# Optimization experiments

Hardware: AMD Instinct MI355X
Metric: run time of the kernel (lower is better)

Reference implementation:

```python
import jax, jax.numpy as jnp
import numpy as np

C = jnp.complex64

def _ry_mat(t):
    c = jnp.cos(t / 2).astype(C)
    s = jnp.sin(t / 2).astype(C)
    return jnp.stack([jnp.stack([c, -s], -1), jnp.stack([s, c], -1)], -2)

def _rx_mat(t):
    c = jnp.cos(t / 2).astype(C)
    s = (-1j) * jnp.sin(t / 2).astype(C)
    return jnp.stack([jnp.stack([c, s], -1), jnp.stack([s, c], -1)], -2)

def _rz_mat(t):
    em = jnp.exp(-1j * (t / 2).astype(C))
    ep = jnp.exp(1j * (t / 2).astype(C))
    z = jnp.zeros_like(em)
    return jnp.stack([jnp.stack([em, z], -1), jnp.stack([z, ep], -1)], -2)

def _apply_1q(psi, gate, w):
    # psi: [bsz, 2^n]; gate: [2,2] (shared) or [bsz,2,2] (per-sample)
    bsz = psi.shape[0]
    s = psi.reshape(bsz, 1 << w, 2, -1)  # wire w isolated on axis 2
    if gate.ndim == 2:
        out = jnp.einsum('ij,bljr->blir', gate, s)
    else:
        out = jnp.einsum('bij,bljr->blir', gate, s)
    return out.reshape(bsz, -1)

def _apply_cnot(psi, c, t):
    bsz = psi.shape[0]
    a, b = min(c, t), max(c, t)
    s = psi.reshape(bsz, 1 << a, 2, 1 << (b - a - 1), 2, -1)
    if c < t:
        # control on axis 2, target on axis 4; after slicing ctrl=1, target -> axis 3
        s = s.at[:, :, 1].set(jnp.flip(s[:, :, 1], axis=3))
    else:
        # control on axis 4, target on axis 2
        s = s.at[:, :, :, :, 1].set(jnp.flip(s[:, :, :, :, 1], axis=2))
    return s.reshape(bsz, -1)

def setup_inputs() -> dict:
    key = jax.random.key(0)
    k1, k2 = jax.random.split(key)
    bsz, n_wires, n_qlayers = 1024, 14, 4
    x_raw = jax.random.normal(k1, (bsz, n_wires), dtype=jnp.float32)
    angles = jax.random.normal(k2, (n_qlayers, n_wires, 3), dtype=jnp.float32) * 0.1
    return {"x_raw": x_raw, "angles": angles}

def reference(x_raw, angles):
    L, n, _ = angles.shape
    bsz = x_raw.shape[0]
    x_enc = jnp.tanh(x_raw[:, :n]) * jnp.pi  # [bsz, n]
    # |0...0> statevector, wire 0 is the most significant bit
    psi = jnp.zeros((bsz, 1 << n), dtype=C).at[:, 0].set(1.0)
    # RY encoding (per-sample angles)
    for w in range(n):
        psi = _apply_1q(psi, _ry_mat(x_enc[:, w]), w)
    # variational layers
    for k in range(L):
        for w in range(n):
            psi = _apply_1q(psi, _rx_mat(angles[k, w, 0]), w)
            psi = _apply_1q(psi, _ry_mat(angles[k, w, 1]), w)
            psi = _apply_1q(psi, _rz_mat(angles[k, w, 2]), w)
        for i in range(n - 1):
            psi = _apply_cnot(psi, i, i + 1)
        psi = _apply_cnot(psi, n - 1, 0)
    # <Z_0>: +|amp|^2 when bit0=0, -|amp|^2 when bit0=1
    p = jnp.abs(psi.reshape(bsz, 2, -1)) ** 2
    return (p[:, 0].sum(-1) - p[:, 1].sum(-1)).astype(jnp.float32)
```

## Files before the change

### kernel.cpp

```cpp
#include <hip/hip_runtime.h>
#include <cmath>
#include <cstdint>

#define NW       14
#define NST      (1 << NW)
#define THREADS  512
#define PRETHR   768
#define NPASS    12
#define WTP      512

typedef _Float16 f16;
typedef _Float16 f16x8 __attribute__((ext_vector_type(8)));
typedef float    f32x4 __attribute__((ext_vector_type(4)));
typedef unsigned short u16;

struct PassArg { u16 Mm[4]; u16 Mt[3]; u16 Mw[3]; };
struct Plan { PassArg ps[NPASS]; u16 initM[14]; u16 measR; u16 _pad; };

__device__ __forceinline__ float2 cmulf(float2 a, float2 b) {
    return make_float2(a.x * b.x - a.y * b.y, a.x * b.y + a.y * b.x);
}
__device__ __host__ __forceinline__ unsigned wtofs(unsigned m, unsigned q01) {
    return (m * 16 + q01 * 8) ^ (((m >> 2) & 1u) << 3);
}

__global__ __launch_bounds__(PRETHR)
void vqc_pre(const float* __restrict__ angles, f16* __restrict__ wt_g,
             float2* __restrict__ u0_g)
{
    __shared__ float2 G[4 * NW * 4];
    const int tid = threadIdx.x;

    if (tid < 4 * NW) {
        const int k = tid / NW, w = tid % NW;
        const float a  = angles[(k * NW + w) * 3 + 0];
        const float bb = angles[(k * NW + w) * 3 + 1];
        const float c  = angles[(k * NW + w) * 3 + 2];
        float sa, ca, sb, cb, sc, cc;
        sincosf(a * 0.5f, &sa, &ca);
        sincosf(bb * 0.5f, &sb, &cb);
        sincosf(c * 0.5f, &sc, &cc);
        float2 m00 = make_float2(cb * ca,  sb * sa);
        float2 m01 = make_float2(-sb * ca, -cb * sa);
        float2 m10 = make_float2(sb * ca,  -cb * sa);
        float2 m11 = make_float2(cb * ca,  -sb * sa);
        const float2 e0 = make_float2(cc, -sc), e1 = make_float2(cc, sc);
        const float2 u00 = cmulf(e0, m00), u01 = cmulf(e0, m01);
        const float2 u10 = cmulf(e1, m10), u11 = cmulf(e1, m11);
        const int gi = (k * NW + w) * 4;
        G[gi + 0] = u00; G[gi + 1] = u01; G[gi + 2] = u10; G[gi + 3] = u11;
        if (k == 0) {
            u0_g[w * 4 + 0] = u00; u0_g[w * 4 + 1] = u01;
            u0_g[w * 4 + 2] = u10; u0_g[w * 4 + 3] = u11;
        }
    }
    __syncthreads();

    {
        const int p = tid >> 6, l6 = tid & 63;
        const int ap = l6 & 15, ahalf = (l6 >> 4) & 1, dup = l6 >> 5;
        const int layer = (p >> 2) + 1, g = p & 3;

        float2 p3;
        if (g == 3) {
            p3 = make_float2((((ap >> 3) & 1) == ahalf) ? 1.f : 0.f, 0.f);
        } else {
            const int wire = 13 - (10 - 4 * g + 3);
            p3 = G[(layer * NW + wire) * 4 + ((ap >> 3) & 1) * 2 + ahalf];
        }
        float2 e0a, e0b, e1a, e1b, e2a, e2b;
        {
            const int r0 = ap & 1, r1 = (ap >> 1) & 1, r2 = (ap >> 2) & 1;
            if (g == 3) {
                const float2* G13 = G + (layer * NW + 13) * 4;
                const float2* G12 = G + (layer * NW + 12) * 4;
                e0a = G13[r0 * 2 + 0]; e0b = G13[r0 * 2 + 1];
                e1a = G12[r1 * 2 + 0]; e1b = G12[r1 * 2 + 1];
                e2a = make_float2(r2 == 0 ? 1.f : 0.f, 0.f);
                e2b = make_float2(r2 == 1 ? 1.f : 0.f, 0.f);
            } else {
                const float2* G0 = G + (layer * NW + (13 - (10 - 4 * g + 0))) * 4;
                const float2* G1 = G + (layer * NW + (13 - (10 - 4 * g + 1))) * 4;
                const float2* G2 = G + (layer * NW + (13 - (10 - 4 * g + 2))) * 4;
                e0a = G0[r0 * 2 + 0]; e0b = G0[r0 * 2 + 1];
                e1a = G1[r1 * 2 + 0]; e1b = G1[r1 * 2 + 1];
                e2a = G2[r2 * 2 + 0]; e2b = G2[r2 * 2 + 1];
            }
        }
        f16x8 frag;
        #pragma unroll
        for (int j2 = 0; j2 < 8; ++j2) {
            float2 v = cmulf(p3, (j2 & 4) ? e2b : e2a);
            v = cmulf(v, (j2 & 2) ? e1b : e1a);
            v = cmulf(v, (j2 & 1) ? e0b : e0a);
            frag[j2] = (f16)(dup ? v.y : v.x);
        }
        *(f16x8*)(wt_g + p * WTP + dup * 256 + wtofs(ap, ahalf)) = frag;
    }
}

__global__ __launch_bounds__(THREADS, 4)
void vqc_kernel(const float* __restrict__ x_raw, const f16* __restrict__ wt_g,
                const float2* __restrict__ u0_g, float* __restrict__ out, Plan pl)
{
    extern __shared__ char smem[];
    f16*    Sh  = (f16*)smem;
    f16*    Wt  = Sh + 2 * NST;
    float2* G0c = (float2*)(Wt + NPASS * WTP);
    float*  red = (float*)(G0c + 2 * NW);

    const int b   = blockIdx.x;
    const int tid = threadIdx.x;
    const int lane = tid & 63, wv = tid >> 6;
    const int q = lane >> 4, m = lane & 15;

    {
        const uint4* src = (const uint4*)wt_g;
        uint4* dst = (uint4*)Wt;
        dst[tid] = src[tid];
        if (tid < 256) dst[512 + tid] = src[512 + tid];
    }
    if (tid < NW) {
        const float xe = tanhf(x_raw[b * NW + tid]) * 3.14159265358979f;
        float se, ce;
        sincosf(xe * 0.5f, &se, &ce);
        const float2 u00 = u0_g[tid * 4 + 0], u01 = u0_g[tid * 4 + 1];
        const float2 u10 = u0_g[tid * 4 + 2], u11 = u0_g[tid * 4 + 3];
        G0c[tid * 2 + 0] = make_float2(u00.x * ce + u01.x * se, u00.y * ce + u01.y * se);
        G0c[tid * 2 + 1] = make_float2(u10.x * ce + u11.x * se, u10.y * ce + u11.y * se);
    }
    __syncthreads();

    {
        float2 common = make_float2(1.f, 0.f);
        #pragma unroll
        for (int bit = 0; bit < 9; ++bit) {
            const int w = 13 - bit;
            const float2 f = ((tid >> bit) & 1) ? G0c[w * 2 + 1] : G0c[w * 2 + 0];
            common = cmulf(common, f);
        }
        unsigned p9 = 0;
        #pragma unroll
        for (int bit = 0; bit < 9; ++bit)
            p9 ^= ((tid >> bit) & 1) ? (unsigned)pl.initM[bit] : 0u;

        const float2 f0a = G0c[4*2+0], f0b = G0c[4*2+1];
        const float2 f1a = G0c[3*2+0], f1b = G0c[3*2+1];
        const float2 f2a = G0c[2*2+0], f2b = G0c[2*2+1];
        const float2 f3a = G0c[1*2+0], f3b = G0c[1*2+1];
        const float2 f4a = G0c[0*2+0], f4b = G0c[0*2+1];

        const unsigned S   = (unsigned)pl.initM[13];
        const unsigned Slo = S & 15u, Hh = S & ~15u;
        const unsigned plo = p9 & 15u, B0 = p9 & ~15u;

        #pragma unroll
        for (int c = 0; c < 2; ++c) {
            const unsigned r = plo ^ (c ? Slo : 0u);
            const bool s0 = ((r       ) & 1u) != 0;
            const bool s1 = (((r) ^ (r >> 1)) & 1u) != 0;
            const bool s2 = (((r >> 1) ^ (r >> 2)) & 1u) != 0;
            const bool s3 = (((r >> 2) ^ (r >> 3)) & 1u) != 0;
            const bool s4 = ((((r >> 3) & 1u) ^ (unsigned)c) != 0);
            const float2 F0[2] = { s0 ? f0b : f0a, s0 ? f0a : f0b };
            const float2 F1[2] = { s1 ? f1b : f1a, s1 ? f1a : f1b };
            const float2 F2[2] = { s2 ? f2b : f2a, s2 ? f2a : f2b };
            const float2 F3[2] = { s3 ? f3b : f3a, s3 ? f3a : f3b };
            const float2 F4[2] = { s4 ? f4b : f4a, s4 ? f4a : f4b };
            const float2 A0 = cmulf(common, F4[0]);
            const float2 A1 = cmulf(common, F4[1]);
            float2 Bt[4];
            Bt[0] = cmulf(A0, F3[0]); Bt[1] = cmulf(A0, F3[1]);
            Bt[2] = cmulf(A1, F3[1]); Bt[3] = cmulf(A1, F3[0]);
            float2 Ct[8];
            #pragma unroll
            for (int o32 = 0; o32 < 4; ++o32) {
                const int o2 = o32 & 1;
                Ct[o32 * 2 + 0] = cmulf(Bt[o32], F2[o2]);
                Ct[o32 * 2 + 1] = cmulf(Bt[o32], F2[1 ^ o2]);
            }
            float2 Gt[4];
            Gt[0] = cmulf(F1[0], F0[0]); Gt[1] = cmulf(F1[1], F0[1]);
            Gt[2] = cmulf(F1[1], F0[0]); Gt[3] = cmulf(F1[0], F0[1]);

            union { f16 h[8]; f16x8 v; } hR[2], hI[2];
            #pragma unroll
            for (int o = 0; o < 16; ++o) {
                const int o0 = o & 1, o1 = (o >> 1) & 1;
                const float2 amp = cmulf(Ct[o >> 1], Gt[o1 * 2 + o0]);
                hR[o >> 3].h[o & 7] = (f16)amp.x;
                hI[o >> 3].h[o & 7] = (f16)amp.y;
            }
            const unsigned bb = B0 ^ (c ? Hh : 0u);
            *(f16x8*)(Sh + bb)           = hR[0].v;
            *(f16x8*)(Sh + bb + 8)       = hR[1].v;
            *(f16x8*)(Sh + NST + bb)     = hI[0].v;
            *(f16x8*)(Sh + NST + bb + 8) = hI[1].v;
        }
    }
    __syncthreads();

    const unsigned plane_off = (unsigned)(q >> 1) << 14;
    const unsigned q01 = (unsigned)(q & 1);
    const f32x4 z4 = {0.f, 0.f, 0.f, 0.f};
    #pragma unroll
    for (int p = 0; p < NPASS; ++p) {
        const PassArg& P = pl.ps[p];
        const unsigned pm = ((m & 1) ? P.Mm[0] : 0) ^ ((m & 2) ? P.Mm[1] : 0)
                          ^ ((m & 4) ? P.Mm[2] : 0) ^ ((m & 8) ? P.Mm[3] : 0);
        const unsigned wb = ((wv & 1) ? P.Mw[0] : 0) ^ ((wv & 2) ? P.Mw[1] : 0)
                          ^ ((wv & 4) ? P.Mw[2] : 0);
        const unsigned b0 = pm ^ wb;
        const f16x8 tr = *(const f16x8*)(Wt + p * WTP +       wtofs((unsigned)m, q01));
        const f16x8 ti = *(const f16x8*)(Wt + p * WTP + 256 + wtofs((unsigned)m, q01));
        const f16x8 bf1 = (q < 2) ? tr : -ti;
        const f16x8 bf2 = (q < 2) ? ti : tr;
        unsigned sw[8];
        f16x8 av[8];
        #pragma unroll
        for (int tt = 0; tt < 8; ++tt) {
            sw[tt] = b0 ^ ((tt & 1) ? P.Mt[0] : 0)
                        ^ ((tt & 2) ? P.Mt[1] : 0)
                        ^ ((tt & 4) ? P.Mt[2] : 0);
            av[tt] = *(const f16x8*)(Sh + plane_off + (sw[tt] ^ (q01 << 3)));
        }
        #pragma unroll
        for (int tt = 0; tt < 8; ++tt) {
            const f32x4 d1 = __builtin_amdgcn_mfma_f32_16x16x32_f16(av[tt], bf1, z4, 0, 0, 0);
            const f32x4 d2 = __builtin_amdgcn_mfma_f32_16x16x32_f16(av[tt], bf2, z4, 0, 0, 0);
            union { f16 h[4]; uint2 u; } c1, c2;
            #pragma unroll
            for (int r = 0; r < 4; ++r) { c1.h[r] = (f16)d1[r]; c2.h[r] = (f16)d2[r]; }
            const unsigned wu = sw[tt] ^ ((unsigned)q << 2);
            *(uint2*)(Sh + wu)       = c1.u;
            *(uint2*)(Sh + NST + wu) = c2.u;
        }
        __syncthreads();
    }

    float acc = 0.f;
    {
        #pragma unroll
        for (int cch = 0; cch < 4; ++cch) {
            const unsigned addr = (unsigned)cch * 4096u + (unsigned)tid * 8u;
            const f16x8 rr = *(const f16x8*)(Sh + addr);
            const f16x8 ii = *(const f16x8*)(Sh + NST + addr);
            const int pb = __popc(addr & (unsigned)pl.measR) & 1;
            #pragma unroll
            for (int e = 0; e < 8; ++e) {
                const float re = (float)rr[e], im = (float)ii[e];
                const float pw = fmaf(re, re, im * im);
                const int sgn = pb ^ (__popc((unsigned)e & (unsigned)pl.measR) & 1);
                acc += sgn ? -pw : pw;
            }
        }
    }
    #pragma unroll
    for (int off = 32; off > 0; off >>= 1) acc += __shfl_down(acc, off);
    if ((tid & 63) == 0) red[wv] = acc;
    __syncthreads();
    if (tid == 0) {
        float s = 0.f;
        #pragma unroll
        for (int i = 0; i < THREADS / 64; ++i) s += red[i];
        out[b] = s;
    }
}

struct GFm { u16 col[14]; };

static unsigned ringp_host(unsigned x) {
    unsigned s = x;
    s ^= s >> 1; s ^= s >> 2; s ^= s >> 4; s ^= s >> 8;
    s &= 0x3FFFu;
    return (s ^ ((s & 1u) << 13)) & 0x3FFFu;
}
static u16 gf_apply(const GFm& m, u16 v) {
    u16 r = 0;
    for (int b = 0; b < 14; ++b) if ((v >> b) & 1) r ^= m.col[b];
    return r;
}
static GFm gf_compose(const GFm& A, const GFm& B) {
    GFm C;
    for (int b = 0; b < 14; ++b) C.col[b] = gf_apply(A, B.col[b]);
    return C;
}
static void rows_from(const GFm& A, u16 r[14]) {
    for (int i = 0; i < 14; ++i) {
        u16 mm = 0;
        for (int b = 0; b < 14; ++b) mm |= (u16)(((A.col[b] >> i) & 1) << b);
        r[i] = mm;
    }
}
static GFm from_rows(const u16 r[14]) {
    GFm A;
    for (int b = 0; b < 14; ++b) {
        u16 c = 0;
        for (int i = 0; i < 14; ++i) c |= (u16)(((r[i] >> b) & 1) << i);
        A.col[b] = c;
    }
    return A;
}
static GFm gf_inv(const GFm& A) {
    u16 M[14], I[14];
    rows_from(A, M);
    for (int i = 0; i < 14; ++i) I[i] = (u16)(1u << i);
    for (int c = 0; c < 14; ++c) {
        int p = c;
        while (p < 14 && !((M[p] >> c) & 1)) ++p;
        if (p == 14) continue;
        u16 t = M[c]; M[c] = M[p]; M[p] = t;
        t = I[c]; I[c] = I[p]; I[p] = t;
        for (int r2 = 0; r2 < 14; ++r2)
            if (r2 != c && ((M[r2] >> c) & 1)) { M[r2] ^= M[c]; I[r2] ^= I[c]; }
    }
    return from_rows(I);
}

static void build_plan(Plan& pl) {
    GFm ring, ringInv;
    for (int b = 0; b < 14; ++b) ring.col[b] = (u16)ringp_host(1u << b);
    ringInv = gf_inv(ring);

    GFm phi;
    for (int j = 0; j < 4; ++j) phi.col[10 + j] = (u16)(1u << j);
    for (int j = 0; j < 4; ++j) phi.col[6 + j]  = (u16)(1u << (4 + j));
    for (int j = 0; j < 4; ++j) phi.col[2 + j]  = (u16)(1u << (8 + j));
    phi.col[0] = (u16)(1u << 12);
    phi.col[1] = (u16)(1u << 13);

    for (int b = 0; b < 14; ++b) pl.initM[b] = gf_apply(phi, ring.col[b]);

    const int gb[4][4] = {{10,11,12,13},{6,7,8,9},{2,3,4,5},{0,1,6,7}};

    for (int p = 0; p < NPASS; ++p) {
        const int g = p & 3;
        u16 uv[4];
        if (g < 3) for (int j = 0; j < 4; ++j) uv[j] = (u16)(1u << gb[g + 1][j]);
        else       for (int j = 0; j < 4; ++j) uv[j] = ringInv.col[10 + j];
        for (int j = 0; j < 4; ++j) pl.ps[p].Mm[j] = gf_apply(phi, uv[j]);

        u16 span[14]; int ns = 0;
        u16 tv[6]; int nt = 0;
        auto tryAdd = [&](u16 v) -> bool {
            bool ch = true;
            while (ch) {
                ch = false;
                for (int i = 0; i < ns; ++i) {
                    const int tb = 31 - __builtin_clz((unsigned)span[i]);
                    if ((v >> tb) & 1) { v ^= span[i]; ch = true; }
                }
            }
            if (!v) return false;
            span[ns++] = v;
            return true;
        };
        for (int j = 0; j < 4; ++j) tryAdd((u16)(1u << gb[g][j]));
        for (int j = 0; j < 4; ++j) tryAdd(uv[j]);
        for (int b2 = 0; b2 < 14 && nt < 6; ++b2)
            if (tryAdd((u16)(1u << b2))) tv[nt++] = (u16)(1u << b2);
        for (int i = 0; i < 3; ++i) pl.ps[p].Mt[i] = gf_apply(phi, tv[i]);
        for (int i = 0; i < 3; ++i) pl.ps[p].Mw[i] = gf_apply(phi, tv[i + 3]);

        GFm Bm;
        for (int j = 0; j < 4; ++j) Bm.col[j]     = (u16)(1u << gb[g][j]);
        for (int j = 0; j < 4; ++j) Bm.col[4 + j] = uv[j];
        for (int i = 0; i < 6; ++i) Bm.col[8 + i] = tv[i];
        GFm Binv = gf_inv(Bm);
        u16 img[14];
        for (int j = 0; j < 4; ++j) img[j]     = pl.ps[p].Mm[j];
        for (int j = 0; j < 4; ++j) img[4 + j] = (u16)(1u << j);
        for (int i = 0; i < 6; ++i) img[8 + i] = gf_apply(phi, tv[i]);
        GFm nphi;
        for (int b2 = 0; b2 < 14; ++b2) {
            const u16 coef = gf_apply(Binv, (u16)(1u << b2));
            u16 v = 0;
            for (int j = 0; j < 14; ++j) if ((coef >> j) & 1) v ^= img[j];
            nphi.col[b2] = v;
        }
        if (g == 3) nphi = gf_compose(nphi, ringInv);
        phi = nphi;
    }

    GFm pinv = gf_inv(phi);
    u16 rows[14];
    rows_from(pinv, rows);
    pl.measR = rows[13];
    pl._pad = 0;
}

struct SwzP { unsigned c4, c5; unsigned char Lc[8]; };

static unsigned proj35(const SwzP& s, u16 v) {
    unsigned a = ((unsigned)v >> 3) & 7u;
    unsigned r = (a & 1u) ? 1u : 0u;
    if (a & 2u) r ^= s.c4;
    if (a & 4u) r ^= s.c5;
    unsigned hb = ((unsigned)v >> 6) & 0xFFu;
    for (int c = 0; c < 8; ++c) if ((hb >> c) & 1u) r ^= s.Lc[c];
    return r & 7u;
}
static int rank3(const unsigned* q, int n) {
    unsigned bas[3] = {0, 0, 0};
    int r = 0;
    for (int j = 0; j < n; ++j) {
        unsigned v = q[j];
        for (int bit = 2; bit >= 0; --bit) {
            if (!((v >> bit) & 1u)) continue;
            if (bas[bit]) { v ^= bas[bit]; continue; }
            bas[bit] = v; ++r; v = 0; break;
        }
    }
    return r;
}
static bool minv_ok(unsigned c4, unsigned c5) {
    const unsigned q[3] = {1u, c4 & 7u, c5 & 7u};
    return rank3(q, 3) == 3;
}
static int score_swz(const SwzP& s, const u16 MmRaw[NPASS][4]) {
    int bad = 0;
    for (int p = 0; p < NPASS; ++p) {
        unsigned q[4];
        for (int j = 0; j < 4; ++j) q[j] = proj35(s, MmRaw[p][j]);
        bad += 3 - rank3(q, 4);
    }
    return bad;
}
static GFm A_from(const SwzP& s) {
    GFm A;
    for (int b = 0; b < 14; ++b) A.col[b] = (u16)(1u << b);
    A.col[4] = (u16)((s.c4 & 7u) << 3);
    A.col[5] = (u16)((s.c5 & 7u) << 3);
    for (int c = 0; c < 8; ++c)
        A.col[6 + c] = (u16)((1u << (6 + c)) ^ (((unsigned)s.Lc[c] & 7u) << 3));
    return A;
}
static void choose_swz(const Plan& raw, GFm& A, GFm& Ainv) {
    u16 MmRaw[NPASS][4];
    for (int p = 0; p < NPASS; ++p)
        for (int j = 0; j < 4; ++j) MmRaw[p][j] = raw.ps[p].Mm[j];

    SwzP best = {2u, 4u, {1, 2, 4, 1, 2, 5, 2, 4}};
    int bestScore = score_swz(best, MmRaw);

    uint64_t rng = 0x9E3779B97F4A7C15ull;
    auto rnd = [&]() -> unsigned {
        rng = rng * 6364136223846793005ull + 1442695040888963407ull;
        return (unsigned)(rng >> 33);
    };
    for (int t = 0; t < 8000 && bestScore > 0; ++t) {
        SwzP s;
        s.c4 = rnd() & 7u; s.c5 = rnd() & 7u;
        if (!minv_ok(s.c4, s.c5)) continue;
        for (int c = 0; c < 8; ++c) s.Lc[c] = (unsigned char)(rnd() & 7u);
        const int sc = score_swz(s, MmRaw);
        if (sc < bestScore) { bestScore = sc; best = s; }
    }
    A = A_from(best);
    Ainv = gf_inv(A);
}
static void fold_A(Plan& pl, const GFm& A, const GFm& Ainv) {
    for (int p = 0; p < NPASS; ++p) {
        for (int j = 0; j < 4; ++j) pl.ps[p].Mm[j] = gf_apply(A, pl.ps[p].Mm[j]);
        for (int j = 0; j < 3; ++j) pl.ps[p].Mt[j] = gf_apply(A, pl.ps[p].Mt[j]);
        for (int j = 0; j < 3; ++j) pl.ps[p].Mw[j] = gf_apply(A, pl.ps[p].Mw[j]);
    }
    for (int b = 0; b < 14; ++b) pl.initM[b] = gf_apply(A, pl.initM[b]);
    const unsigned r = pl.measR;
    u16 nr = 0;
    for (int b = 0; b < 14; ++b)
        if (__builtin_popcount(r & (unsigned)Ainv.col[b]) & 1) nr |= (u16)(1u << b);
    pl.measR = nr;
}

extern "C" void kernel_launch(void* const* d_in, const int* in_sizes, int n_in,
                              void* d_out, int out_size, void* d_ws, size_t ws_size,
                              hipStream_t stream) {
    const float* x_raw  = (const float*)d_in[0];
    const float* angles = (const float*)d_in[1];
    float* out = (float*)d_out;
    const int bsz = in_sizes[0] / NW;

    Plan pl;
    build_plan(pl);
    GFm A, Ainv;
    choose_swz(pl, A, Ainv);
    fold_A(pl, A, Ainv);

    f16*    wt_g = (f16*)d_ws;
    float2* u0_g = (float2*)((char*)d_ws + (size_t)NPASS * WTP * sizeof(f16));

    vqc_pre<<<dim3(1), dim3(PRETHR), 0, stream>>>(angles, wt_g, u0_g);

    const size_t lds = (size_t)2 * NST * sizeof(f16)
                     + (size_t)NPASS * WTP * sizeof(f16)
                     + (size_t)(2 * NW) * sizeof(float2)
                     + (size_t)(THREADS / 64) * sizeof(float);
    (void)hipFuncSetAttribute((const void*)vqc_kernel,
                              hipFuncAttributeMaxDynamicSharedMemorySize, (int)lds);
    vqc_kernel<<<dim3(bsz), dim3(THREADS), lds, stream>>>(x_raw, wt_g, u0_g, out, pl);
}
```

Baseline: 107.8 us.

## Fuse gate precompute into main kernel and double block size to 1024 threads

Removes the separate single-block precompute kernel. Each block now computes the gate matrices and MFMA weight tiles itself in shared memory, which drops one launch and the global round trip through the workspace. The block grows to 1024 threads (16 waves), so each thread handles half as many tiles per pass: the tile-vector/wave-vector split moves from 3/3 to 2/4 and the init and measurement loops are reworked to match. The cost is redundant gate computation in every block, extra shared memory, and a launch-bounds occupancy hint that may not be achievable at this LDS footprint.

```diff
diff --git a/kernel.cpp b/kernel.cpp
--- a/kernel.cpp
+++ b/kernel.cpp
@@ -4,8 +4,7 @@
 
 #define NW       14
 #define NST      (1 << NW)
-#define THREADS  512
-#define PRETHR   768
+#define THREADS  1024
 #define NPASS    12
 #define WTP      512
 
@@ -14,7 +13,7 @@
 typedef float    f32x4 __attribute__((ext_vector_type(4)));
 typedef unsigned short u16;
 
-struct PassArg { u16 Mm[4]; u16 Mt[3]; u16 Mw[3]; };
+struct PassArg { u16 Mm[4]; u16 Mt[2]; u16 Mw[4]; };
 struct Plan { PassArg ps[NPASS]; u16 initM[14]; u16 measR; u16 _pad; };
 
 __device__ __forceinline__ float2 cmulf(float2 a, float2 b) {
@@ -24,12 +23,21 @@
     return (m * 16 + q01 * 8) ^ (((m >> 2) & 1u) << 3);
 }
 
-__global__ __launch_bounds__(PRETHR)
-void vqc_pre(const float* __restrict__ angles, f16* __restrict__ wt_g,
-             float2* __restrict__ u0_g)
+__global__ __launch_bounds__(THREADS, 8)
+void vqc_kernel(const float* __restrict__ x_raw, const float* __restrict__ angles,
+                float* __restrict__ out, Plan pl)
 {
-    __shared__ float2 G[4 * NW * 4];
+    extern __shared__ char smem[];
+    f16*    Sh  = (f16*)smem;
+    f16*    Wt  = Sh + 2 * NST;
+    float2* Gg  = (float2*)(Wt + NPASS * WTP);
+    float2* G0c = Gg + 4 * NW * 4;
+    float*  red = (float*)(G0c + 2 * NW);
+
+    const int b   = blockIdx.x;
     const int tid = threadIdx.x;
+    const int lane = tid & 63, wv = tid >> 6;
+    const int q = lane >> 4, m = lane & 15;
 
     if (tid < 4 * NW) {
         const int k = tid / NW, w = tid % NW;
@@ -48,15 +56,18 @@
         const float2 u00 = cmulf(e0, m00), u01 = cmulf(e0, m01);
         const float2 u10 = cmulf(e1, m10), u11 = cmulf(e1, m11);
         const int gi = (k * NW + w) * 4;
-        G[gi + 0] = u00; G[gi + 1] = u01; G[gi + 2] = u10; G[gi + 3] = u11;
+        Gg[gi + 0] = u00; Gg[gi + 1] = u01; Gg[gi + 2] = u10; Gg[gi + 3] = u11;
         if (k == 0) {
-            u0_g[w * 4 + 0] = u00; u0_g[w * 4 + 1] = u01;
-            u0_g[w * 4 + 2] = u10; u0_g[w * 4 + 3] = u11;
+            const float xe = tanhf(x_raw[b * NW + w]) * 3.14159265358979f;
+            float se, ce;
+            sincosf(xe * 0.5f, &se, &ce);
+            G0c[w * 2 + 0] = make_float2(u00.x * ce + u01.x * se, u00.y * ce + u01.y * se);
+            G0c[w * 2 + 1] = make_float2(u10.x * ce + u11.x * se, u10.y * ce + u11.y * se);
         }
     }
     __syncthreads();
 
-    {
+    if (tid < 768) {
         const int p = tid >> 6, l6 = tid & 63;
         const int ap = l6 & 15, ahalf = (l6 >> 4) & 1, dup = l6 >> 5;
         const int layer = (p >> 2) + 1, g = p & 3;
@@ -66,22 +77,22 @@
             p3 = make_float2((((ap >> 3) & 1) == ahalf) ? 1.f : 0.f, 0.f);
         } else {
             const int wire = 13 - (10 - 4 * g + 3);
-            p3 = G[(layer * NW + wire) * 4 + ((ap >> 3) & 1) * 2 + ahalf];
+            p3 = Gg[(layer * NW + wire) * 4 + ((ap >> 3) & 1) * 2 + ahalf];
         }
         float2 e0a, e0b, e1a, e1b, e2a, e2b;
         {
             const int r0 = ap & 1, r1 = (ap >> 1) & 1, r2 = (ap >> 2) & 1;
             if (g == 3) {
-                const float2* G13 = G + (layer * NW + 13) * 4;
-                const float2* G12 = G + (layer * NW + 12) * 4;
+                const float2* G13 = Gg + (layer * NW + 13) * 4;
+                const float2* G12 = Gg + (layer * NW + 12) * 4;
                 e0a = G13[r0 * 2 + 0]; e0b = G13[r0 * 2 + 1];
                 e1a = G12[r1 * 2 + 0]; e1b = G12[r1 * 2 + 1];
                 e2a = make_float2(r2 == 0 ? 1.f : 0.f, 0.f);
                 e2b = make_float2(r2 == 1 ? 1.f : 0.f, 0.f);
             } else {
-                const float2* G0 = G + (layer * NW + (13 - (10 - 4 * g + 0))) * 4;
-                const float2* G1 = G + (layer * NW + (13 - (10 - 4 * g + 1))) * 4;
-                const float2* G2 = G + (layer * NW + (13 - (10 - 4 * g + 2))) * 4;
+                const float2* G0 = Gg + (layer * NW + (13 - (10 - 4 * g + 0))) * 4;
+                const float2* G1 = Gg + (layer * NW + (13 - (10 - 4 * g + 1))) * 4;
+                const float2* G2 = Gg + (layer * NW + (13 - (10 - 4 * g + 2))) * 4;
                 e0a = G0[r0 * 2 + 0]; e0b = G0[r0 * 2 + 1];
                 e1a = G1[r1 * 2 + 0]; e1b = G1[r1 * 2 + 1];
                 e2a = G2[r2 * 2 + 0]; e2b = G2[r2 * 2 + 1];
@@ -95,41 +106,8 @@
             v = cmulf(v, (j2 & 1) ? e0b : e0a);
             frag[j2] = (f16)(dup ? v.y : v.x);
         }
-        *(f16x8*)(wt_g + p * WTP + dup * 256 + wtofs(ap, ahalf)) = frag;
-    }
-}
-
-__global__ __launch_bounds__(THREADS, 4)
-void vqc_kernel(const float* __restrict__ x_raw, const f16* __restrict__ wt_g,
-                const float2* __restrict__ u0_g, float* __restrict__ out, Plan pl)
-{
-    extern __shared__ char smem[];
-    f16*    Sh  = (f16*)smem;
-    f16*    Wt  = Sh + 2 * NST;
-    float2* G0c = (float2*)(Wt + NPASS * WTP);
-    float*  red = (float*)(G0c + 2 * NW);
-
-    const int b   = blockIdx.x;
-    const int tid = threadIdx.x;
-    const int lane = tid & 63, wv = tid >> 6;
-    const int q = lane >> 4, m = lane & 15;
-
-    {
-        const uint4* src = (const uint4*)wt_g;
-        uint4* dst = (uint4*)Wt;
-        dst[tid] = src[tid];
-        if (tid < 256) dst[512 + tid] = src[512 + tid];
-    }
-    if (tid < NW) {
-        const float xe = tanhf(x_raw[b * NW + tid]) * 3.14159265358979f;
-        float se, ce;
-        sincosf(xe * 0.5f, &se, &ce);
-        const float2 u00 = u0_g[tid * 4 + 0], u01 = u0_g[tid * 4 + 1];
-        const float2 u10 = u0_g[tid * 4 + 2], u11 = u0_g[tid * 4 + 3];
-        G0c[tid * 2 + 0] = make_float2(u00.x * ce + u01.x * se, u00.y * ce + u01.y * se);
-        G0c[tid * 2 + 1] = make_float2(u10.x * ce + u11.x * se, u10.y * ce + u11.y * se);
-    }
-    __syncthreads();
+        *(f16x8*)(Wt + p * WTP + dup * 256 + wtofs(ap, ahalf)) = frag;
+    }
 
     {
         float2 common = make_float2(1.f, 0.f);
@@ -139,63 +117,49 @@
             const float2 f = ((tid >> bit) & 1) ? G0c[w * 2 + 1] : G0c[w * 2 + 0];
             common = cmulf(common, f);
         }
-        unsigned p9 = 0;
+        common = cmulf(common, (tid & 512) ? G0c[0 * 2 + 1] : G0c[0 * 2 + 0]);
+        unsigned p10 = 0;
         #pragma unroll
         for (int bit = 0; bit < 9; ++bit)
-            p9 ^= ((tid >> bit) & 1) ? (unsigned)pl.initM[bit] : 0u;
-
-        const float2 f0a = G0c[4*2+0], f0b = G0c[4*2+1];
-        const float2 f1a = G0c[3*2+0], f1b = G0c[3*2+1];
-        const float2 f2a = G0c[2*2+0], f2b = G0c[2*2+1];
-        const float2 f3a = G0c[1*2+0], f3b = G0c[1*2+1];
-        const float2 f4a = G0c[0*2+0], f4b = G0c[0*2+1];
-
-        const unsigned S   = (unsigned)pl.initM[13];
-        const unsigned Slo = S & 15u, Hh = S & ~15u;
-        const unsigned plo = p9 & 15u, B0 = p9 & ~15u;
+            p10 ^= ((tid >> bit) & 1) ? (unsigned)pl.initM[bit] : 0u;
+        if (tid & 512) p10 ^= (unsigned)pl.initM[13];
+        const unsigned t9 = (unsigned)pl.initM[9];
+
+        const float2 w4a = G0c[4*2+0], w4b = G0c[4*2+1];
+        const float2 w3a = G0c[3*2+0], w3b = G0c[3*2+1];
+        const float2 w2a = G0c[2*2+0], w2b = G0c[2*2+1];
+        const float2 w1a = G0c[1*2+0], w1b = G0c[1*2+1];
 
         #pragma unroll
         for (int c = 0; c < 2; ++c) {
-            const unsigned r = plo ^ (c ? Slo : 0u);
-            const bool s0 = ((r       ) & 1u) != 0;
-            const bool s1 = (((r) ^ (r >> 1)) & 1u) != 0;
-            const bool s2 = (((r >> 1) ^ (r >> 2)) & 1u) != 0;
-            const bool s3 = (((r >> 2) ^ (r >> 3)) & 1u) != 0;
-            const bool s4 = ((((r >> 3) & 1u) ^ (unsigned)c) != 0);
-            const float2 F0[2] = { s0 ? f0b : f0a, s0 ? f0a : f0b };
-            const float2 F1[2] = { s1 ? f1b : f1a, s1 ? f1a : f1b };
-            const float2 F2[2] = { s2 ? f2b : f2a, s2 ? f2a : f2b };
-            const float2 F3[2] = { s3 ? f3b : f3a, s3 ? f3a : f3b };
-            const float2 F4[2] = { s4 ? f4b : f4a, s4 ? f4a : f4b };
-            const float2 A0 = cmulf(common, F4[0]);
-            const float2 A1 = cmulf(common, F4[1]);
-            float2 Bt[4];
-            Bt[0] = cmulf(A0, F3[0]); Bt[1] = cmulf(A0, F3[1]);
-            Bt[2] = cmulf(A1, F3[1]); Bt[3] = cmulf(A1, F3[0]);
-            float2 Ct[8];
-            #pragma unroll
-            for (int o32 = 0; o32 < 4; ++o32) {
-                const int o2 = o32 & 1;
-                Ct[o32 * 2 + 0] = cmulf(Bt[o32], F2[o2]);
-                Ct[o32 * 2 + 1] = cmulf(Bt[o32], F2[1 ^ o2]);
-            }
-            float2 Gt[4];
-            Gt[0] = cmulf(F1[0], F0[0]); Gt[1] = cmulf(F1[1], F0[1]);
-            Gt[2] = cmulf(F1[1], F0[0]); Gt[3] = cmulf(F1[0], F0[1]);
-
-            union { f16 h[8]; f16x8 v; } hR[2], hI[2];
-            #pragma unroll
-            for (int o = 0; o < 16; ++o) {
-                const int o0 = o & 1, o1 = (o >> 1) & 1;
-                const float2 amp = cmulf(Ct[o >> 1], Gt[o1 * 2 + o0]);
-                hR[o >> 3].h[o & 7] = (f16)amp.x;
-                hI[o >> 3].h[o & 7] = (f16)amp.y;
-            }
-            const unsigned bb = B0 ^ (c ? Hh : 0u);
-            *(f16x8*)(Sh + bb)           = hR[0].v;
-            *(f16x8*)(Sh + bb + 8)       = hR[1].v;
-            *(f16x8*)(Sh + NST + bb)     = hI[0].v;
-            *(f16x8*)(Sh + NST + bb + 8) = hI[1].v;
+            const unsigned ac = p10 ^ (c ? t9 : 0u);
+            const unsigned r = ac & 7u;
+            const unsigned base = ac & ~7u;
+            const bool sA = ((r ^ (unsigned)c) & 1u) != 0;
+            const bool sB = ((r ^ (r >> 1)) & 1u) != 0;
+            const bool sC = (((r >> 1) ^ (r >> 2)) & 1u) != 0;
+            const bool sD = ((r >> 2) & 1u) != 0;
+            const float2 A_[2] = { sA ? w4b : w4a, sA ? w4a : w4b };
+            const float2 B_[2] = { sB ? w3b : w3a, sB ? w3a : w3b };
+            const float2 C_[2] = { sC ? w2b : w2a, sC ? w2a : w2b };
+            const float2 D_[2] = { sD ? w1b : w1a, sD ? w1a : w1b };
+            const float2 U0  = cmulf(common, A_[0]), U1  = cmulf(common, A_[1]);
+            const float2 W00 = cmulf(U0, B_[0]),     W01 = cmulf(U0, B_[1]);
+            const float2 W10 = cmulf(U1, B_[1]),     W11 = cmulf(U1, B_[0]);
+            const float2 V00 = cmulf(C_[0], D_[0]),  V01 = cmulf(C_[1], D_[1]);
+            const float2 V10 = cmulf(C_[1], D_[0]),  V11 = cmulf(C_[0], D_[1]);
+            union { f16 h[8]; f16x8 v; } hR, hI;
+            float2 amp;
+            amp = cmulf(W00, V00); hR.h[0] = (f16)amp.x; hI.h[0] = (f16)amp.y;
+            amp = cmulf(W10, V00); hR.h[1] = (f16)amp.x; hI.h[1] = (f16)amp.y;
+            amp = cmulf(W01, V10); hR.h[2] = (f16)amp.x; hI.h[2] = (f16)amp.y;
+            amp = cmulf(W11, V10); hR.h[3] = (f16)amp.x; hI.h[3] = (f16)amp.y;
+            amp = cmulf(W00, V01); hR.h[4] = (f16)amp.x; hI.h[4] = (f16)amp.y;
+            amp = cmulf(W10, V01); hR.h[5] = (f16)amp.x; hI.h[5] = (f16)amp.y;
+            amp = cmulf(W01, V11); hR.h[6] = (f16)amp.x; hI.h[6] = (f16)amp.y;
+            amp = cmulf(W11, V11); hR.h[7] = (f16)amp.x; hI.h[7] = (f16)amp.y;
+            *(f16x8*)(Sh + base)       = hR.v;
+            *(f16x8*)(Sh + NST + base) = hI.v;
         }
     }
     __syncthreads();
@@ -209,23 +173,22 @@
         const unsigned pm = ((m & 1) ? P.Mm[0] : 0) ^ ((m & 2) ? P.Mm[1] : 0)
                           ^ ((m & 4) ? P.Mm[2] : 0) ^ ((m & 8) ? P.Mm[3] : 0);
         const unsigned wb = ((wv & 1) ? P.Mw[0] : 0) ^ ((wv & 2) ? P.Mw[1] : 0)
-                          ^ ((wv & 4) ? P.Mw[2] : 0);
+                          ^ ((wv & 4) ? P.Mw[2] : 0) ^ ((wv & 8) ? P.Mw[3] : 0);
         const unsigned b0 = pm ^ wb;
         const f16x8 tr = *(const f16x8*)(Wt + p * WTP +       wtofs((unsigned)m, q01));
         const f16x8 ti = *(const f16x8*)(Wt + p * WTP + 256 + wtofs((unsigned)m, q01));
         const f16x8 bf1 = (q < 2) ? tr : -ti;
         const f16x8 bf2 = (q < 2) ? ti : tr;
-        unsigned sw[8];
-        f16x8 av[8];
-        #pragma unroll
-        for (int tt = 0; tt < 8; ++tt) {
+        unsigned sw[4];
+        f16x8 av[4];
+        #pragma unroll
+        for (int tt = 0; tt < 4; ++tt) {
             sw[tt] = b0 ^ ((tt & 1) ? P.Mt[0] : 0)
-                        ^ ((tt & 2) ? P.Mt[1] : 0)
-                        ^ ((tt & 4) ? P.Mt[2] : 0);
+                        ^ ((tt & 2) ? P.Mt[1] : 0);
             av[tt] = *(const f16x8*)(Sh + plane_off + (sw[tt] ^ (q01 << 3)));
         }
         #pragma unroll
-        for (int tt = 0; tt < 8; ++tt) {
+        for (int tt = 0; tt < 4; ++tt) {
             const f32x4 d1 = __builtin_amdgcn_mfma_f32_16x16x32_f16(av[tt], bf1, z4, 0, 0, 0);
             const f32x4 d2 = __builtin_amdgcn_mfma_f32_16x16x32_f16(av[tt], bf2, z4, 0, 0, 0);
             union { f16 h[4]; uint2 u; } c1, c2;
@@ -240,17 +203,17 @@
 
     float acc = 0.f;
     {
-        #pragma unroll
-        for (int cch = 0; cch < 4; ++cch) {
-            const unsigned addr = (unsigned)cch * 4096u + (unsigned)tid * 8u;
-            const f16x8 rr = *(const f16x8*)(Sh + addr);
-            const f16x8 ii = *(const f16x8*)(Sh + NST + addr);
-            const int pb = __popc(addr & (unsigned)pl.measR) & 1;
+        const unsigned base = (unsigned)tid * 16u;
+        const int pb = __popc(base & (unsigned)pl.measR) & 1;
+        #pragma unroll
+        for (int half = 0; half < 2; ++half) {
+            const f16x8 rr = *(const f16x8*)(Sh + base + half * 8);
+            const f16x8 ii = *(const f16x8*)(Sh + NST + base + half * 8);
             #pragma unroll
             for (int e = 0; e < 8; ++e) {
                 const float re = (float)rr[e], im = (float)ii[e];
                 const float pw = fmaf(re, re, im * im);
-                const int sgn = pb ^ (__popc((unsigned)e & (unsigned)pl.measR) & 1);
+                const int sgn = pb ^ (__popc((unsigned)(half * 8 + e) & (unsigned)pl.measR) & 1);
                 acc += sgn ? -pw : pw;
             }
         }
@@ -359,8 +322,8 @@
         for (int j = 0; j < 4; ++j) tryAdd(uv[j]);
         for (int b2 = 0; b2 < 14 && nt < 6; ++b2)
             if (tryAdd((u16)(1u << b2))) tv[nt++] = (u16)(1u << b2);
-        for (int i = 0; i < 3; ++i) pl.ps[p].Mt[i] = gf_apply(phi, tv[i]);
-        for (int i = 0; i < 3; ++i) pl.ps[p].Mw[i] = gf_apply(phi, tv[i + 3]);
+        for (int i = 0; i < 2; ++i) pl.ps[p].Mt[i] = gf_apply(phi, tv[i]);
+        for (int i = 0; i < 4; ++i) pl.ps[p].Mw[i] = gf_apply(phi, tv[i + 2]);
 
         GFm Bm;
         for (int j = 0; j < 4; ++j) Bm.col[j]     = (u16)(1u << gb[g][j]);
@@ -462,8 +425,8 @@
 static void fold_A(Plan& pl, const GFm& A, const GFm& Ainv) {
     for (int p = 0; p < NPASS; ++p) {
         for (int j = 0; j < 4; ++j) pl.ps[p].Mm[j] = gf_apply(A, pl.ps[p].Mm[j]);
-        for (int j = 0; j < 3; ++j) pl.ps[p].Mt[j] = gf_apply(A, pl.ps[p].Mt[j]);
-        for (int j = 0; j < 3; ++j) pl.ps[p].Mw[j] = gf_apply(A, pl.ps[p].Mw[j]);
+        for (int j = 0; j < 2; ++j) pl.ps[p].Mt[j] = gf_apply(A, pl.ps[p].Mt[j]);
+        for (int j = 0; j < 4; ++j) pl.ps[p].Mw[j] = gf_apply(A, pl.ps[p].Mw[j]);
     }
     for (int b = 0; b < 14; ++b) pl.initM[b] = gf_apply(A, pl.initM[b]);
     const unsigned r = pl.measR;
@@ -487,16 +450,12 @@
     choose_swz(pl, A, Ainv);
     fold_A(pl, A, Ainv);
 
-    f16*    wt_g = (f16*)d_ws;
-    float2* u0_g = (float2*)((char*)d_ws + (size_t)NPASS * WTP * sizeof(f16));
-
-    vqc_pre<<<dim3(1), dim3(PRETHR), 0, stream>>>(angles, wt_g, u0_g);
-
     const size_t lds = (size_t)2 * NST * sizeof(f16)
                      + (size_t)NPASS * WTP * sizeof(f16)
+                     + (size_t)(4 * NW * 4) * sizeof(float2)
                      + (size_t)(2 * NW) * sizeof(float2)
                      + (size_t)(THREADS / 64) * sizeof(float);
     (void)hipFuncSetAttribute((const void*)vqc_kernel,
                               hipFuncAttributeMaxDynamicSharedMemorySize, (int)lds);
-    vqc_kernel<<<dim3(bsz), dim3(THREADS), lds, stream>>>(x_raw, wt_g, u0_g, out, pl);
-}
+    vqc_kernel<<<dim3(bsz), dim3(THREADS), lds, stream>>>(x_raw, angles, out, pl);
+}
```

New measurement: 118.3 us. +9.8%, slower.

## Fuse gate-table precompute into main kernel and merge LDS stores via ds_write2st64

Applied to the files above, without the earlier changes.

Removes the separate single-block preprocessing kernel. Each block now computes the gate matrices and the fp16 MFMA weight tables directly into LDS, which eliminates one launch and the global round-trip of the tables. In exchange, every block repeats the small trig and table-building work, and LDS use grows by the gate array. The two fp16 output stores per MFMA (real and imaginary planes, 64*64*2 bytes apart) are also merged into one inline-asm ds_write2st64_b64 instruction.

```diff
diff --git a/kernel.cpp b/kernel.cpp
--- a/kernel.cpp
+++ b/kernel.cpp
@@ -5,7 +5,6 @@
 #define NW       14
 #define NST      (1 << NW)
 #define THREADS  512
-#define PRETHR   768
 #define NPASS    12
 #define WTP      512
 
@@ -24,12 +23,21 @@
     return (m * 16 + q01 * 8) ^ (((m >> 2) & 1u) << 3);
 }
 
-__global__ __launch_bounds__(PRETHR)
-void vqc_pre(const float* __restrict__ angles, f16* __restrict__ wt_g,
-             float2* __restrict__ u0_g)
+__global__ __launch_bounds__(THREADS, 4)
+void vqc_kernel(const float* __restrict__ x_raw, const float* __restrict__ angles,
+                float* __restrict__ out, Plan pl)
 {
-    __shared__ float2 G[4 * NW * 4];
+    extern __shared__ char smem[];
+    f16*    Sh  = (f16*)smem;
+    f16*    Wt  = Sh + 2 * NST;
+    float2* Gg  = (float2*)(Wt + NPASS * WTP);
+    float2* G0c = Gg + 4 * NW * 4;
+    float*  red = (float*)(G0c + 2 * NW);
+
+    const int b   = blockIdx.x;
     const int tid = threadIdx.x;
+    const int lane = tid & 63, wv = tid >> 6;
+    const int q = lane >> 4, m = lane & 15;
 
     if (tid < 4 * NW) {
         const int k = tid / NW, w = tid % NW;
@@ -48,16 +56,19 @@
         const float2 u00 = cmulf(e0, m00), u01 = cmulf(e0, m01);
         const float2 u10 = cmulf(e1, m10), u11 = cmulf(e1, m11);
         const int gi = (k * NW + w) * 4;
-        G[gi + 0] = u00; G[gi + 1] = u01; G[gi + 2] = u10; G[gi + 3] = u11;
+        Gg[gi + 0] = u00; Gg[gi + 1] = u01; Gg[gi + 2] = u10; Gg[gi + 3] = u11;
         if (k == 0) {
-            u0_g[w * 4 + 0] = u00; u0_g[w * 4 + 1] = u01;
-            u0_g[w * 4 + 2] = u10; u0_g[w * 4 + 3] = u11;
+            const float xe = tanhf(x_raw[b * NW + w]) * 3.14159265358979f;
+            float se, ce;
+            sincosf(xe * 0.5f, &se, &ce);
+            G0c[w * 2 + 0] = make_float2(u00.x * ce + u01.x * se, u00.y * ce + u01.y * se);
+            G0c[w * 2 + 1] = make_float2(u10.x * ce + u11.x * se, u10.y * ce + u11.y * se);
         }
     }
     __syncthreads();
 
-    {
-        const int p = tid >> 6, l6 = tid & 63;
+    for (int slot = tid; slot < 768; slot += THREADS) {
+        const int p = slot >> 6, l6 = slot & 63;
         const int ap = l6 & 15, ahalf = (l6 >> 4) & 1, dup = l6 >> 5;
         const int layer = (p >> 2) + 1, g = p & 3;
 
@@ -66,22 +77,22 @@
             p3 = make_float2((((ap >> 3) & 1) == ahalf) ? 1.f : 0.f, 0.f);
         } else {
             const int wire = 13 - (10 - 4 * g + 3);
-            p3 = G[(layer * NW + wire) * 4 + ((ap >> 3) & 1) * 2 + ahalf];
+            p3 = Gg[(layer * NW + wire) * 4 + ((ap >> 3) & 1) * 2 + ahalf];
         }
         float2 e0a, e0b, e1a, e1b, e2a, e2b;
         {
             const int r0 = ap & 1, r1 = (ap >> 1) & 1, r2 = (ap >> 2) & 1;
             if (g == 3) {
-                const float2* G13 = G + (layer * NW + 13) * 4;
-                const float2* G12 = G + (layer * NW + 12) * 4;
+                const float2* G13 = Gg + (layer * NW + 13) * 4;
+                const float2* G12 = Gg + (layer * NW + 12) * 4;
                 e0a = G13[r0 * 2 + 0]; e0b = G13[r0 * 2 + 1];
                 e1a = G12[r1 * 2 + 0]; e1b = G12[r1 * 2 + 1];
                 e2a = make_float2(r2 == 0 ? 1.f : 0.f, 0.f);
                 e2b = make_float2(r2 == 1 ? 1.f : 0.f, 0.f);
             } else {
-                const float2* G0 = G + (layer * NW + (13 - (10 - 4 * g + 0))) * 4;
-                const float2* G1 = G + (layer * NW + (13 - (10 - 4 * g + 1))) * 4;
-                const float2* G2 = G + (layer * NW + (13 - (10 - 4 * g + 2))) * 4;
+                const float2* G0 = Gg + (layer * NW + (13 - (10 - 4 * g + 0))) * 4;
+                const float2* G1 = Gg + (layer * NW + (13 - (10 - 4 * g + 1))) * 4;
+                const float2* G2 = Gg + (layer * NW + (13 - (10 - 4 * g + 2))) * 4;
                 e0a = G0[r0 * 2 + 0]; e0b = G0[r0 * 2 + 1];
                 e1a = G1[r1 * 2 + 0]; e1b = G1[r1 * 2 + 1];
                 e2a = G2[r2 * 2 + 0]; e2b = G2[r2 * 2 + 1];
@@ -95,41 +106,8 @@
             v = cmulf(v, (j2 & 1) ? e0b : e0a);
             frag[j2] = (f16)(dup ? v.y : v.x);
         }
-        *(f16x8*)(wt_g + p * WTP + dup * 256 + wtofs(ap, ahalf)) = frag;
-    }
-}
-
-__global__ __launch_bounds__(THREADS, 4)
-void vqc_kernel(const float* __restrict__ x_raw, const f16* __restrict__ wt_g,
-                const float2* __restrict__ u0_g, float* __restrict__ out, Plan pl)
-{
-    extern __shared__ char smem[];
-    f16*    Sh  = (f16*)smem;
-    f16*    Wt  = Sh + 2 * NST;
-    float2* G0c = (float2*)(Wt + NPASS * WTP);
-    float*  red = (float*)(G0c + 2 * NW);
-
-    const int b   = blockIdx.x;
-    const int tid = threadIdx.x;
-    const int lane = tid & 63, wv = tid >> 6;
-    const int q = lane >> 4, m = lane & 15;
-
-    {
-        const uint4* src = (const uint4*)wt_g;
-        uint4* dst = (uint4*)Wt;
-        dst[tid] = src[tid];
-        if (tid < 256) dst[512 + tid] = src[512 + tid];
-    }
-    if (tid < NW) {
-        const float xe = tanhf(x_raw[b * NW + tid]) * 3.14159265358979f;
-        float se, ce;
-        sincosf(xe * 0.5f, &se, &ce);
-        const float2 u00 = u0_g[tid * 4 + 0], u01 = u0_g[tid * 4 + 1];
-        const float2 u10 = u0_g[tid * 4 + 2], u11 = u0_g[tid * 4 + 3];
-        G0c[tid * 2 + 0] = make_float2(u00.x * ce + u01.x * se, u00.y * ce + u01.y * se);
-        G0c[tid * 2 + 1] = make_float2(u10.x * ce + u11.x * se, u10.y * ce + u11.y * se);
-    }
-    __syncthreads();
+        *(f16x8*)(Wt + p * WTP + dup * 256 + wtofs(ap, ahalf)) = frag;
+    }
 
     {
         float2 common = make_float2(1.f, 0.f);
@@ -228,12 +206,13 @@
         for (int tt = 0; tt < 8; ++tt) {
             const f32x4 d1 = __builtin_amdgcn_mfma_f32_16x16x32_f16(av[tt], bf1, z4, 0, 0, 0);
             const f32x4 d2 = __builtin_amdgcn_mfma_f32_16x16x32_f16(av[tt], bf2, z4, 0, 0, 0);
-            union { f16 h[4]; uint2 u; } c1, c2;
+            union { f16 h[4]; unsigned long long u; } c1, c2;
             #pragma unroll
             for (int r = 0; r < 4; ++r) { c1.h[r] = (f16)d1[r]; c2.h[r] = (f16)d2[r]; }
             const unsigned wu = sw[tt] ^ ((unsigned)q << 2);
-            *(uint2*)(Sh + wu)       = c1.u;
-            *(uint2*)(Sh + NST + wu) = c2.u;
+            const unsigned lds_addr = (unsigned)(uintptr_t)(Sh + wu);
+            asm volatile("ds_write2st64_b64 %0, %1, %2 offset0:0 offset1:64"
+                         :: "v"(lds_addr), "v"(c1.u), "v"(c2.u) : "memory");
         }
         __syncthreads();
     }
@@ -487,16 +466,12 @@
     choose_swz(pl, A, Ainv);
     fold_A(pl, A, Ainv);
 
-    f16*    wt_g = (f16*)d_ws;
-    float2* u0_g = (float2*)((char*)d_ws + (size_t)NPASS * WTP * sizeof(f16));
-
-    vqc_pre<<<dim3(1), dim3(PRETHR), 0, stream>>>(angles, wt_g, u0_g);
-
     const size_t lds = (size_t)2 * NST * sizeof(f16)
                      + (size_t)NPASS * WTP * sizeof(f16)
+                     + (size_t)(4 * NW * 4) * sizeof(float2)
                      + (size_t)(2 * NW) * sizeof(float2)
                      + (size_t)(THREADS / 64) * sizeof(float);
     (void)hipFuncSetAttribute((const void*)vqc_kernel,
                               hipFuncAttributeMaxDynamicSharedMemorySize, (int)lds);
-    vqc_kernel<<<dim3(bsz), dim3(THREADS), lds, stream>>>(x_raw, wt_g, u0_g, out, pl);
-}
+    vqc_kernel<<<dim3(bsz), dim3(THREADS), lds, stream>>>(x_raw, angles, out, pl);
+}
```

Result: no change. 109.6 us (+1.7%).
